# Kernel tuning notes

Measured on AMD Instinct MI355X. Metric: run time of the kernel, lower is better.

Reference implementation:

```python
import jax, jax.numpy as jnp
import numpy as np

B, T, C = 2, 2048, 2048
N_HEAD, N_KV_HEAD = 16, 4
HEAD_DIM = C // N_HEAD  # 128
EPS = 1e-6


def rms_norm(x):
    # no learned scale, normalize over head_dim (last axis)
    return x * jax.lax.rsqrt(jnp.mean(jnp.square(x), axis=-1, keepdims=True) + EPS)


def apply_rotary_emb(x, cos, sin):
    # x: [B, T, H, D]; cos/sin: [T, D/2]  (rotate-half RoPE)
    x1, x2 = jnp.split(x, 2, axis=-1)
    c = cos[None, :, None, :]
    s = sin[None, :, None, :]
    return jnp.concatenate([x1 * c - x2 * s, x1 * s + x2 * c], axis=-1)


def setup_inputs() -> dict:
    key = jax.random.key(0)
    ks = jax.random.split(key, 6)
    x = jax.random.normal(ks[0], (B, T, C), dtype=jnp.float32)
    # real rotary tables: theta = 10000^{-2i/D}
    inv_freq = 1.0 / (10000.0 ** (jnp.arange(0, HEAD_DIM, 2, dtype=jnp.float32) / HEAD_DIM))
    angles = jnp.arange(T, dtype=jnp.float32)[:, None] * inv_freq[None, :]  # [T, D/2]
    cos, sin = jnp.cos(angles), jnp.sin(angles)
    std = 0.02
    Wq = jax.random.normal(ks[1], (C, N_HEAD * HEAD_DIM), dtype=jnp.float32) * std
    Wk = jax.random.normal(ks[2], (C, N_KV_HEAD * HEAD_DIM), dtype=jnp.float32) * std
    Wv = jax.random.normal(ks[3], (C, N_KV_HEAD * HEAD_DIM), dtype=jnp.float32) * std
    Wp = jax.random.normal(ks[4], (C, C), dtype=jnp.float32) * std
    return {"x": x, "cos": cos, "sin": sin, "Wq": Wq, "Wk": Wk, "Wv": Wv, "Wp": Wp}


def reference(x, cos, sin, Wq, Wk, Wv, Wp):
    Bx, Tx, Cx = x.shape
    q = (x @ Wq).reshape(Bx, Tx, N_HEAD, HEAD_DIM)
    k = (x @ Wk).reshape(Bx, Tx, N_KV_HEAD, HEAD_DIM)
    v = (x @ Wv).reshape(Bx, Tx, N_KV_HEAD, HEAD_DIM)
    q = rms_norm(apply_rotary_emb(q, cos, sin))
    k = rms_norm(apply_rotary_emb(k, cos, sin))
    # module scales q by 1/sqrt(D) AND nn.dot_product_attention scales again
    q = q * (1.0 / jnp.sqrt(HEAD_DIM))
    # GQA head repeat
    n_rep = N_HEAD // N_KV_HEAD
    k = jnp.repeat(k, n_rep, axis=2)  # [B, T, H, D]
    v = jnp.repeat(v, n_rep, axis=2)
    scores = jnp.einsum("bthd,bshd->bhts", q, k) / jnp.sqrt(jnp.asarray(HEAD_DIM, x.dtype))
    causal = jnp.tril(jnp.ones((Tx, Tx), dtype=bool))  # key <= query
    scores = jnp.where(causal[None, None, :, :], scores, jnp.finfo(scores.dtype).min)
    probs = jax.nn.softmax(scores, axis=-1)
    y = jnp.einsum("bhts,bshd->bthd", probs, v).reshape(Bx, Tx, Cx)
    return y @ Wp
```

## Files before the change

### kernel.cpp

```cpp
#include <hip/hip_runtime.h>
#include <hip/hip_bf16.h>
#include <math.h>

#define B_  2
#define T_  2048
#define C_  2048
#define NH_ 16
#define NKV_ 4
#define HD_ 128
#define NREP_ (NH_/NKV_)

#define QKVLD 3072
#define KOFF  2048
#define VOFF  2560

#define QSCALE 0.01127105500694502f

#if defined(__has_builtin)
# if __has_builtin(__builtin_amdgcn_exp2f)
#  define EXP2F(x) __builtin_amdgcn_exp2f(x)
# else
#  define EXP2F(x) exp2f(x)
# endif
#else
# define EXP2F(x) exp2f(x)
#endif

typedef __bf16 bf16x8 __attribute__((ext_vector_type(8)));
typedef float  f32x4  __attribute__((ext_vector_type(4)));
typedef float  f32x16 __attribute__((ext_vector_type(16)));

__device__ inline void gload_lds16(const void* g, void* l) {
    __builtin_amdgcn_global_load_lds((const __attribute__((address_space(1))) void*)g,
                                     (__attribute__((address_space(3))) void*)l, 16, 0, 0);
}

__global__ __launch_bounds__(256) void prep(const float* __restrict__ x,
                                            const float* __restrict__ Wq,
                                            const float* __restrict__ Wk,
                                            const float* __restrict__ Wv,
                                            const float* __restrict__ Wp,
                                            __bf16* __restrict__ xb,
                                            __bf16* __restrict__ wqkvT,
                                            __bf16* __restrict__ wpT)
{
    __shared__ float tl[32][33];
    const int bx  = blockIdx.x;
    const int tid = threadIdx.x;

    if (bx < 4096) {
        size_t i = ((size_t)bx * 256 + tid) * 8;
        float4 a = *(const float4*)&x[i];
        float4 b = *(const float4*)&x[i + 4];
        union { __bf16 h[8]; uint4 u; } pk;
        pk.h[0] = (__bf16)a.x; pk.h[1] = (__bf16)a.y; pk.h[2] = (__bf16)a.z; pk.h[3] = (__bf16)a.w;
        pk.h[4] = (__bf16)b.x; pk.h[5] = (__bf16)b.y; pk.h[6] = (__bf16)b.z; pk.h[7] = (__bf16)b.w;
        *(uint4*)&xb[i] = pk.u;
        return;
    }

    const float* src;
    int ncols, c0, dr0, k0;
    if (bx < 10240) {
        int r  = bx - 4096;
        int ct = r % 96;
        k0 = (r / 96) * 32;
        if (ct < 64)      { src = Wq; ncols = 2048; c0 = ct * 32;        dr0 = ct * 32; }
        else if (ct < 80) { src = Wk; ncols = 512;  c0 = (ct - 64) * 32; dr0 = KOFF + (ct - 64) * 32; }
        else              { src = Wv; ncols = 512;  c0 = (ct - 80) * 32; dr0 = VOFF + (ct - 80) * 32; }
    } else {
        int r  = bx - 10240;
        src = Wp; ncols = 2048;
        c0  = (r & 63) * 32; dr0 = c0;
        k0  = (r >> 6) * 32;
    }
    __bf16* dst = (bx < 10240) ? wqkvT : wpT;

    int rr = tid >> 3;
    int c4 = (tid & 7) * 4;
    float4 v = *(const float4*)&src[(size_t)(k0 + rr) * ncols + c0 + c4];
    tl[rr][c4] = v.x; tl[rr][c4 + 1] = v.y; tl[rr][c4 + 2] = v.z; tl[rr][c4 + 3] = v.w;
    __syncthreads();
    union { __bf16 h[4]; uint2 u; } pk;
#pragma unroll
    for (int j = 0; j < 4; ++j) pk.h[j] = (__bf16)tl[c4 + j][rr];
    *(uint2*)&dst[(size_t)(dr0 + rr) * 2048 + k0 + c4] = pk.u;
}

template<typename TOUT>
__global__ __launch_bounds__(256) void gemm_bt(const __bf16* __restrict__ A,
                                               const __bf16* __restrict__ Bt,
                                               TOUT* __restrict__ C,
                                               int M, int N, int K, int ldc)
{
    __shared__ __bf16 As[2][128 * 32];
    __shared__ __bf16 Bs[2][128 * 32];

    const int tid  = threadIdx.x;
    const int wv   = tid >> 6;
    const int lane = tid & 63;
    const int grp  = lane >> 4;
    const int id16 = lane & 15;
    const int wr   = wv >> 1;
    const int wc   = wv & 1;

    const int row0 = blockIdx.y * 128;
    const int col0 = blockIdx.x * 128;

    const int sm = tid >> 2;
    const int sk = (tid & 3) << 3;

    const __bf16* ga0 = A  + (size_t)(row0 + sm) * K + sk;
    const __bf16* ga1 = A  + (size_t)(row0 + 64 + sm) * K + sk;
    const __bf16* gb0 = Bt + (size_t)(col0 + sm) * K + sk;
    const __bf16* gb1 = Bt + (size_t)(col0 + 64 + sm) * K + sk;

    f32x4 acc[4][4];
    const f32x4 fz = {0.f, 0.f, 0.f, 0.f};
#pragma unroll
    for (int i = 0; i < 4; ++i)
#pragma unroll
        for (int j = 0; j < 4; ++j) acc[i][j] = fz;

    const int nk = K >> 5;

    {
        __bf16* a0 = &As[0][wv << 9];
        __bf16* b0 = &Bs[0][wv << 9];
        gload_lds16(ga0, a0);
        gload_lds16(ga1, a0 + 2048);
        gload_lds16(gb0, b0);
        gload_lds16(gb1, b0 + 2048);
    }

    for (int kt = 0; kt < nk; ++kt) {
        const int bufc = kt & 1;
        asm volatile("s_waitcnt vmcnt(0)" ::: "memory");
        __syncthreads();

        if (kt + 1 < nk) {
            const int kb = (kt + 1) << 5;
            __bf16* a0 = &As[1 - bufc][wv << 9];
            __bf16* b0 = &Bs[1 - bufc][wv << 9];
            gload_lds16(ga0 + kb, a0);
            gload_lds16(ga1 + kb, a0 + 2048);
            gload_lds16(gb0 + kb, b0);
            gload_lds16(gb1 + kb, b0 + 2048);
        }

        bf16x8 af[4], bfr[4];
#pragma unroll
        for (int i = 0; i < 4; ++i)
            af[i] = *(const bf16x8*)&As[bufc][((wr << 6) + (i << 4) + id16) * 32 + (grp << 3)];
#pragma unroll
        for (int j = 0; j < 4; ++j)
            bfr[j] = *(const bf16x8*)&Bs[bufc][((wc << 6) + (j << 4) + id16) * 32 + (grp << 3)];
#pragma unroll
        for (int i = 0; i < 4; ++i)
#pragma unroll
            for (int j = 0; j < 4; ++j)
                acc[i][j] = __builtin_amdgcn_mfma_f32_16x16x32_bf16(af[i], bfr[j], acc[i][j], 0, 0, 0);
    }

#pragma unroll
    for (int i = 0; i < 4; ++i) {
        int gr = row0 + (wr << 6) + (i << 4) + (grp << 2);
#pragma unroll
        for (int j = 0; j < 4; ++j) {
            int gc = col0 + (wc << 6) + (j << 4) + id16;
#pragma unroll
            for (int r = 0; r < 4; ++r) {
                if constexpr (sizeof(TOUT) == 4)
                    C[(size_t)(gr + r) * ldc + gc] = acc[i][j][r];
                else
                    C[(size_t)(gr + r) * ldc + gc] = (TOUT)acc[i][j][r];
            }
        }
    }
}

__global__ __launch_bounds__(256) void rope_vt(__bf16* __restrict__ qkv,
                                               const float* __restrict__ cosb,
                                               const float* __restrict__ sinb,
                                               __bf16* __restrict__ vt)
{
    __shared__ __bf16 tl[32][HD_ + 8];
    const int bx  = blockIdx.x;
    const int tid = threadIdx.x;

    if (bx < 20480) {
        int gw   = bx * 4 + (tid >> 6);
        int lane = tid & 63;
        int bt = gw / 20;
        int hd = gw % 20;
        int t  = bt & (T_ - 1);
        float scale = (hd < 16) ? QSCALE : 1.0f;

        __bf16* p = qkv + (size_t)bt * QKVLD + hd * HD_;
        float c = cosb[t * 64 + lane];
        float s = sinb[t * 64 + lane];
        float x1 = (float)p[lane];
        float x2 = (float)p[lane + 64];
        float r1 = x1 * c - x2 * s;
        float r2 = x1 * s + x2 * c;
        float ss = r1 * r1 + r2 * r2;
#pragma unroll
        for (int off = 32; off; off >>= 1) ss += __shfl_xor(ss, off, 64);
        float inv = rsqrtf(ss * (1.f / 128.f) + 1e-6f) * scale;
        p[lane]      = (__bf16)(r1 * inv);
        p[lane + 64] = (__bf16)(r2 * inv);
        return;
    }
    {
        int vbx = bx - 20480;
        int st  = vbx & 63;
        int bkv = vbx >> 6;
        int b = bkv >> 2, kv = bkv & 3;
        int s0 = st << 5;
        {
            int s = tid >> 3;
            int d = (tid & 7) << 4;
            const __bf16* src = qkv + (size_t)(b * T_ + s0 + s) * QKVLD + VOFF + kv * HD_ + d;
            *(bf16x8*)&tl[s][d]     = *(const bf16x8*)src;
            *(bf16x8*)&tl[s][d + 8] = *(const bf16x8*)(src + 8);
        }
        __syncthreads();
        {
            int d  = tid >> 1;
            int sh = (tid & 1) << 4;
            __bf16 tmp[16];
#pragma unroll
            for (int j = 0; j < 16; ++j) tmp[j] = tl[sh + j][d];
            __bf16* dst = vt + ((size_t)(b * NKV_ + kv) * HD_ + d) * T_ + s0 + sh;
            *(bf16x8*)dst       = *(bf16x8*)&tmp[0];
            *(bf16x8*)(dst + 8) = *(bf16x8*)&tmp[8];
        }
    }
}

__global__ __launch_bounds__(256, 2) void attn32(const __bf16* __restrict__ qkv,
                                                 const __bf16* __restrict__ vbT,
                                                 __bf16* __restrict__ y,
                                                 float* __restrict__ pOA,
                                                 float* __restrict__ pOB,
                                                 float* __restrict__ pLA,
                                                 float* __restrict__ pLB)
{
    __shared__ __bf16 Ks[2][64 * 128];
    __shared__ __bf16 Vs[2][64 * 128];

    const int tid  = threadIdx.x;
    const int wv   = tid >> 6;
    const int lane = tid & 63;
    const int l31  = lane & 31;
    const int h32  = lane >> 5;

    const int bx   = blockIdx.x;
    const int b    = (bx >> 2) & 1;
    const int kv   = bx & 3;
    const int m    = bx >> 3;
    const int hh   = m & 3;
    const int role = (m >> 2) & 1;
    const int p    = m >> 3;
    const int h    = kv * 4 + hh;
    const int bh   = b * 16 + h;
    const int slot = p * 32 + bh;

    const int hi  = 15 - p;
    const int lo  = p;
    const int tts = role ? (15 - 2 * p) : 99;

    auto KT = [&](int t) { return role ? (t < tts ? 17 + t : t - tts) : t; };

    int qw0 = hi * 128 + wv * 32;
    int qme = qw0 + l31;

    uint koff[4], voff[4];
#pragma unroll
    for (int i = 0; i < 4; ++i) {
        int r  = (wv * 4 + i) * 4 + (lane >> 4);
        int c  = lane & 15;
        int cs = c ^ (r & 15);
        koff[i] = (uint)(r * (QKVLD * 2) + cs * 16);
        int d   = r + ((cs >> 3) << 6);
        voff[i] = (uint)(d * (T_ * 2) + (cs & 7) * 16);
    }
    const char* kg = (const char*)(qkv + (size_t)b * T_ * QKVLD + KOFF + kv * HD_);
    const char* vg = (const char*)(vbT + ((size_t)(b * NKV_ + kv) * HD_) * T_);

    uint off8[8];
#pragma unroll
    for (int s = 0; s < 8; ++s)
        off8[s] = (uint)(l31 * 256 + ((((s << 1) + h32) ^ (l31 & 15)) << 4));

#define STAGE(BUF, KN)                                                        \
    {                                                                         \
        const char* kp = kg + (size_t)(KN) * (64 * QKVLD * 2);                \
        const char* vp = vg + (size_t)(KN) * (64 * 2);                        \
        __bf16* kl = &Ks[BUF][(wv * 4) * 512];                                \
        __bf16* vl = &Vs[BUF][(wv * 4) * 512];                                \
        _Pragma("unroll")                                                     \
        for (int i = 0; i < 4; ++i) gload_lds16(kp + koff[i], kl + i * 512);  \
        _Pragma("unroll")                                                     \
        for (int i = 0; i < 4; ++i) gload_lds16(vp + voff[i], vl + i * 512);  \
    }

    bf16x8 qf[8], qf2[8];
    {
        const __bf16* qp = qkv + (size_t)(b * T_ + hi * 128 + wv * 32 + l31) * QKVLD + h * HD_ + h32 * 8;
#pragma unroll
        for (int s = 0; s < 8; ++s) qf[s] = *(const bf16x8*)(qp + s * 16);
        const __bf16* qp2 = qkv + (size_t)(b * T_ + lo * 128 + wv * 32 + l31) * QKVLD + h * HD_ + h32 * 8;
#pragma unroll
        for (int s = 0; s < 8; ++s) qf2[s] = *(const bf16x8*)(qp2 + s * 16);
    }

    f32x16 o[4];
#pragma unroll
    for (int dt = 0; dt < 4; ++dt)
#pragma unroll
        for (int r = 0; r < 16; ++r) o[dt][r] = 0.f;
    float l_p = 0.f;

#define STORE_PARTIAL(PO, PL)                                                   \
    {                                                                           \
        float lsum = l_p + __shfl_xor(l_p, 32, 64);                             \
        int qloc = wv * 32 + l31;                                               \
        float* po = (PO) + ((size_t)slot * 128 + qloc) * 128;                   \
        _Pragma("unroll")                                                       \
        for (int dt = 0; dt < 4; ++dt)                                          \
            _Pragma("unroll")                                                   \
            for (int g = 0; g < 4; ++g) {                                       \
                float4 f = {o[dt][4 * g + 0], o[dt][4 * g + 1],                 \
                            o[dt][4 * g + 2], o[dt][4 * g + 3]};                \
                *(float4*)&po[dt * 32 + 8 * g + 4 * h32] = f;                   \
            }                                                                   \
        if (h32 == 0) (PL)[slot * 128 + qloc] = lsum;                           \
    }

#define TILE_BODY(TT, BUFC)                                                     \
    {                                                                           \
        const int tt_ = (TT);                                                   \
        asm volatile("s_waitcnt vmcnt(0)" ::: "memory");                        \
        __syncthreads();                                                        \
        if (tt_ + 1 < 17) { int kn_ = KT(tt_ + 1); STAGE(1 - (BUFC), kn_); }    \
        if (role && tt_ == tts) {                                               \
            STORE_PARTIAL(pOB, pLB);                                            \
            _Pragma("unroll")                                                   \
            for (int dt = 0; dt < 4; ++dt)                                      \
                _Pragma("unroll")                                               \
                for (int r = 0; r < 16; ++r) o[dt][r] = 0.f;                    \
            l_p = 0.f;                                                          \
            _Pragma("unroll")                                                   \
            for (int s = 0; s < 8; ++s) qf[s] = qf2[s];                         \
            qw0 = lo * 128 + wv * 32;                                           \
            qme = qw0 + l31;                                                    \
        }                                                                       \
        const int s0 = KT(tt_) << 6;                                            \
        if (s0 <= qw0 + 31) {                                                   \
            const char* Kb = (const char*)&Ks[BUFC][0];                         \
            const char* Vb = (const char*)&Vs[BUFC][0];                         \
            f32x16 S0, S1;                                                      \
            _Pragma("unroll")                                                   \
            for (int r = 0; r < 16; ++r) { S0[r] = 0.f; S1[r] = 0.f; }          \
            __builtin_amdgcn_s_setprio(1);                                      \
            _Pragma("unroll")                                                   \
            for (int s = 0; s < 8; ++s) {                                       \
                bf16x8 kf0 = *(const bf16x8*)(Kb + off8[s]);                    \
                bf16x8 kf1 = *(const bf16x8*)(Kb + off8[s] + 8192);             \
                S0 = __builtin_amdgcn_mfma_f32_32x32x16_bf16(kf0, qf[s], S0, 0, 0, 0); \
                S1 = __builtin_amdgcn_mfma_f32_32x32x16_bf16(kf1, qf[s], S1, 0, 0, 0); \
            }                                                                   \
            __builtin_amdgcn_s_setprio(0);                                      \
            const bool domask = (s0 + 63 > qw0);                                \
            uint w[16];                                                         \
            _Pragma("unroll")                                                   \
            for (int i = 0; i < 8; ++i) {                                       \
                const int r0 = 2 * i;                                           \
                float e0 = EXP2F(S0[r0]);                                       \
                float e1 = EXP2F(S0[r0 + 1]);                                   \
                if (domask) {                                                   \
                    int k0 = s0 + (r0 & 3) + 8 * (r0 >> 2) + 4 * h32;           \
                    if (k0     > qme) e0 = 0.f;                                 \
                    if (k0 + 1 > qme) e1 = 0.f;                                 \
                }                                                               \
                l_p += e0 + e1;                                                 \
                union { __bf16 h2[2]; uint u; } pk;                             \
                pk.h2[0] = (__bf16)e0; pk.h2[1] = (__bf16)e1;                   \
                w[i] = pk.u;                                                    \
            }                                                                   \
            _Pragma("unroll")                                                   \
            for (int i = 0; i < 8; ++i) {                                       \
                const int r0 = 2 * i;                                           \
                float e0 = EXP2F(S1[r0]);                                       \
                float e1 = EXP2F(S1[r0 + 1]);                                   \
                if (domask) {                                                   \
                    int k0 = s0 + 32 + (r0 & 3) + 8 * (r0 >> 2) + 4 * h32;      \
                    if (k0     > qme) e0 = 0.f;                                 \
                    if (k0 + 1 > qme) e1 = 0.f;                                 \
                }                                                               \
                l_p += e0 + e1;                                                 \
                union { __bf16 h2[2]; uint u; } pk;                             \
                pk.h2[0] = (__bf16)e0; pk.h2[1] = (__bf16)e1;                   \
                w[8 + i] = pk.u;                                                \
            }                                                                   \
            union U8 { uint u[4]; bf16x8 v; };                                  \
            bf16x8 pf[4];                                                       \
            _Pragma("unroll")                                                   \
            for (int ks = 0; ks < 4; ++ks) {                                    \
                const int bsel = ((ks >> 1) << 3) + ((ks & 1) << 2);            \
                uint a0 = w[bsel],     b0 = w[bsel + 2];                        \
                uint a1 = w[bsel + 1], b1 = w[bsel + 3];                        \
                asm("v_permlane32_swap_b32 %0, %1" : "+v"(a0), "+v"(b0));       \
                asm("v_permlane32_swap_b32 %0, %1" : "+v"(a1), "+v"(b1));       \
                U8 t;                                                           \
                t.u[0] = a0; t.u[1] = a1; t.u[2] = b0; t.u[3] = b1;             \
                pf[ks] = t.v;                                                   \
            }                                                                   \
            __builtin_amdgcn_s_setprio(1);                                      \
            _Pragma("unroll")                                                   \
            for (int dt = 0; dt < 4; ++dt) {                                    \
                const int ab = (dt >> 1) << 2;                                  \
                const int hf = (dt & 1) * 8192;                                 \
                _Pragma("unroll")                                               \
                for (int ks = 0; ks < 4; ++ks) {                                \
                    bf16x8 vf = *(const bf16x8*)(Vb + off8[ab + ks] + hf);      \
                    o[dt] = __builtin_amdgcn_mfma_f32_32x32x16_bf16(vf, pf[ks], o[dt], 0, 0, 0); \
                }                                                               \
            }                                                                   \
            __builtin_amdgcn_s_setprio(0);                                      \
        }                                                                       \
    }

    STAGE(0, KT(0));

    for (int tt = 0; tt < 16; tt += 2) {
        TILE_BODY(tt, 0);
        TILE_BODY(tt + 1, 1);
    }
    TILE_BODY(16, 0);

    if (role == 0) {
        STORE_PARTIAL(pOA, pLA);
    } else {
        float l  = l_p + __shfl_xor(l_p, 32, 64);
        float inv = 1.f / l;
        __bf16* yp = y + (size_t)(b * T_ + qw0 + l31) * C_ + h * HD_;
#pragma unroll
        for (int dt = 0; dt < 4; ++dt)
#pragma unroll
            for (int g = 0; g < 4; ++g) {
                union { __bf16 h4[4]; uint2 u; } pk;
#pragma unroll
                for (int e = 0; e < 4; ++e) pk.h4[e] = (__bf16)(o[dt][4 * g + e] * inv);
                *(uint2*)&yp[dt * 32 + 8 * g + 4 * h32] = pk.u;
            }
    }
#undef TILE_BODY
#undef STORE_PARTIAL
#undef STAGE
}

__global__ __launch_bounds__(256) void attn_combine(const float* __restrict__ pOA,
                                                    const float* __restrict__ pOB,
                                                    const float* __restrict__ pLA,
                                                    const float* __restrict__ pLB,
                                                    __bf16* __restrict__ y)
{
    int slot = blockIdx.x;
    int p  = slot >> 5, bh = slot & 31;
    int b  = bh >> 4,   h  = bh & 15;
    int hi = 15 - p;
    int t  = threadIdx.x;
    int q  = t >> 1;
    int dh = (t & 1) << 6;

    float inv = 1.f / (pLA[slot * 128 + q] + pLB[slot * 128 + q]);
    size_t base = ((size_t)slot * 128 + q) * 128 + dh;
    __bf16* yp = y + (size_t)(b * T_ + hi * 128 + q) * C_ + h * HD_ + dh;
#pragma unroll
    for (int d0 = 0; d0 < 64; d0 += 8) {
        float4 a0 = *(const float4*)&pOA[base + d0];
        float4 a1 = *(const float4*)&pOA[base + d0 + 4];
        float4 b0 = *(const float4*)&pOB[base + d0];
        float4 b1 = *(const float4*)&pOB[base + d0 + 4];
        union { __bf16 h8[8]; uint4 u; } pk;
        pk.h8[0] = (__bf16)((a0.x + b0.x) * inv);
        pk.h8[1] = (__bf16)((a0.y + b0.y) * inv);
        pk.h8[2] = (__bf16)((a0.z + b0.z) * inv);
        pk.h8[3] = (__bf16)((a0.w + b0.w) * inv);
        pk.h8[4] = (__bf16)((a1.x + b1.x) * inv);
        pk.h8[5] = (__bf16)((a1.y + b1.y) * inv);
        pk.h8[6] = (__bf16)((a1.z + b1.z) * inv);
        pk.h8[7] = (__bf16)((a1.w + b1.w) * inv);
        *(uint4*)&yp[d0] = pk.u;
    }
}

extern "C" void kernel_launch(void* const* d_in, const int* in_sizes, int n_in,
                              void* d_out, int out_size, void* d_ws, size_t ws_size,
                              hipStream_t stream)
{
    const float* x    = (const float*)d_in[0];
    const float* cosb = (const float*)d_in[1];
    const float* sinb = (const float*)d_in[2];
    const float* Wq   = (const float*)d_in[3];
    const float* Wk   = (const float*)d_in[4];
    const float* Wv   = (const float*)d_in[5];
    const float* Wp   = (const float*)d_in[6];
    float* out = (float*)d_out;

    const int M = B_ * T_;

    char* w = (char*)d_ws;
    __bf16* xb    = (__bf16*)w;  w += (size_t)M * C_ * 2;
    __bf16* qkv   = (__bf16*)w;  w += (size_t)M * QKVLD * 2;
    __bf16* wqkvT = (__bf16*)w;  w += (size_t)QKVLD * C_ * 2;
    __bf16* wpT   = (__bf16*)w;  w += (size_t)C_ * C_ * 2;
    __bf16* vt    = (__bf16*)w;  w += (size_t)M * NKV_ * HD_ * 2;
    __bf16* y     = (__bf16*)w;  w += (size_t)M * C_ * 2;
    float*  pOB   = (float*)w;
    float*  pOA   = (float*)xb;
    float*  pLA   = (float*)wqkvT;
    float*  pLB   = pLA + 8 * 32 * 128;

    prep<<<14336, 256, 0, stream>>>(x, Wq, Wk, Wv, Wp, xb, wqkvT, wpT);

    gemm_bt<__bf16><<<dim3(QKVLD / 128, M / 128), 256, 0, stream>>>(xb, wqkvT, qkv, M, QKVLD, C_, QKVLD);

    rope_vt<<<20992, 256, 0, stream>>>(qkv, cosb, sinb, vt);

    attn32<<<512, 256, 0, stream>>>(qkv, vt, y, pOA, pOB, pLA, pLB);
    attn_combine<<<256, 256, 0, stream>>>(pOA, pOB, pLA, pLB, y);

    gemm_bt<float><<<dim3(C_ / 128, M / 128), 256, 0, stream>>>(y, wpT, out, M, C_, C_, C_);
}
```

Before: 310.3 us.

## Use 256x256-tile GEMM with 8 waves for the QKV projection

Adds a new bf16 MFMA GEMM kernel with 256x256 output tiles, K-step 64, 512 threads, double-buffered direct global-to-LDS loads, and an XOR-swizzled LDS layout. The QKV projection now launches this kernel in place of the 128x128 tile kernel. The larger tile raises arithmetic intensity and cuts global traffic per FLOP. The cost is a much smaller grid (12x16 = 192 blocks on a GPU with many CUs, so under one wave) and one block per CU because of the heavy LDS and register use.

```diff
diff --git a/kernel.cpp b/kernel.cpp
--- a/kernel.cpp
+++ b/kernel.cpp
@@ -85,6 +85,124 @@
 #pragma unroll
     for (int j = 0; j < 4; ++j) pk.h[j] = (__bf16)tl[c4 + j][rr];
     *(uint2*)&dst[(size_t)(dr0 + rr) * 2048 + k0 + c4] = pk.u;
+}
+
+template<typename TOUT>
+__global__ __launch_bounds__(512, 1) void gemm256(const __bf16* __restrict__ A,
+                                                  const __bf16* __restrict__ Bt,
+                                                  TOUT* __restrict__ C,
+                                                  int M, int N, int K, int ldc)
+{
+    __shared__ __bf16 As[2][256 * 64];
+    __shared__ __bf16 Bs[2][256 * 64];
+
+    const int tid  = threadIdx.x;
+    const int wv   = tid >> 6;
+    const int lane = tid & 63;
+    const int grp  = lane >> 4;
+    const int id16 = lane & 15;
+    const int wr   = wv >> 2;
+    const int wc   = wv & 3;
+
+    const int row0 = blockIdx.y * 256;
+    const int col0 = blockIdx.x * 256;
+
+    const int srow = lane >> 3;
+    const int cs16 = (((lane & 7) ^ srow) << 4);
+    const __bf16* gA = A  + (size_t)(row0 + wv * 8 + srow) * K;
+    const __bf16* gB = Bt + (size_t)(col0 + wv * 8 + srow) * K;
+
+    const int aBase = (wr * 128 + id16) * 64;
+    const int bBase = (wc * 64  + id16) * 64;
+    int physe[2];
+#pragma unroll
+    for (int ks = 0; ks < 2; ++ks)
+        physe[ks] = (((ks << 2) + grp) ^ (id16 & 7)) << 3;
+
+    f32x4 acc[8][4];
+    const f32x4 fz = {0.f, 0.f, 0.f, 0.f};
+#pragma unroll
+    for (int i = 0; i < 8; ++i)
+#pragma unroll
+        for (int j = 0; j < 4; ++j) acc[i][j] = fz;
+
+    const int NK = K >> 6;
+
+#define STAGE256(BUF, KT)                                                      \
+    {                                                                          \
+        const int kb_ = (KT) << 6;                                             \
+        _Pragma("unroll")                                                      \
+        for (int i = 0; i < 4; ++i)                                            \
+            gload_lds16((const char*)(gA + (size_t)i * 64 * K + kb_) + cs16,   \
+                        &As[BUF][(i * 64 + wv * 8) * 64]);                     \
+        _Pragma("unroll")                                                      \
+        for (int i = 0; i < 4; ++i)                                            \
+            gload_lds16((const char*)(gB + (size_t)i * 64 * K + kb_) + cs16,   \
+                        &Bs[BUF][(i * 64 + wv * 8) * 64]);                     \
+    }
+
+#define TILE256(KT, BUF)                                                       \
+    {                                                                          \
+        if ((KT) == NK - 1) { asm volatile("s_waitcnt vmcnt(0)" ::: "memory"); } \
+        else                { asm volatile("s_waitcnt vmcnt(8)" ::: "memory"); } \
+        __builtin_amdgcn_s_barrier();                                          \
+        _Pragma("unroll")                                                      \
+        for (int p = 0; p < 4; ++p) {                                          \
+            const int mh = p >> 1, nq = p & 1;                                 \
+            bf16x8 af[4][2], bfv[2][2];                                        \
+            _Pragma("unroll")                                                  \
+            for (int s = 0; s < 4; ++s)                                        \
+                _Pragma("unroll")                                              \
+                for (int ks = 0; ks < 2; ++ks)                                 \
+                    af[s][ks] = *(const bf16x8*)&As[BUF][aBase + (mh * 4 + s) * 1024 + physe[ks]]; \
+            _Pragma("unroll")                                                  \
+            for (int s = 0; s < 2; ++s)                                        \
+                _Pragma("unroll")                                              \
+                for (int ks = 0; ks < 2; ++ks)                                 \
+                    bfv[s][ks] = *(const bf16x8*)&Bs[BUF][bBase + (nq * 2 + s) * 1024 + physe[ks]]; \
+            __builtin_amdgcn_s_setprio(1);                                     \
+            _Pragma("unroll")                                                  \
+            for (int s = 0; s < 4; ++s)                                        \
+                _Pragma("unroll")                                              \
+                for (int n = 0; n < 2; ++n)                                    \
+                    _Pragma("unroll")                                          \
+                    for (int ks = 0; ks < 2; ++ks)                             \
+                        acc[mh * 4 + s][nq * 2 + n] =                          \
+                            __builtin_amdgcn_mfma_f32_16x16x32_bf16(af[s][ks], bfv[n][ks], \
+                                                                    acc[mh * 4 + s][nq * 2 + n], 0, 0, 0); \
+            __builtin_amdgcn_s_setprio(0);                                     \
+            __builtin_amdgcn_s_barrier();                                      \
+        }                                                                      \
+        asm volatile("s_waitcnt lgkmcnt(0)" ::: "memory");                     \
+        __builtin_amdgcn_s_barrier();                                          \
+        if ((KT) + 2 < NK) STAGE256(BUF, (KT) + 2);                            \
+    }
+
+    STAGE256(0, 0);
+    STAGE256(1, 1);
+
+    for (int kt = 0; kt < NK; kt += 2) {
+        TILE256(kt, 0);
+        TILE256(kt + 1, 1);
+    }
+
+#pragma unroll
+    for (int mf = 0; mf < 8; ++mf) {
+        int gr = row0 + wr * 128 + mf * 16 + grp * 4;
+#pragma unroll
+        for (int nf = 0; nf < 4; ++nf) {
+            int gc = col0 + wc * 64 + nf * 16 + id16;
+#pragma unroll
+            for (int r = 0; r < 4; ++r) {
+                if constexpr (sizeof(TOUT) == 4)
+                    C[(size_t)(gr + r) * ldc + gc] = acc[mf][nf][r];
+                else
+                    C[(size_t)(gr + r) * ldc + gc] = (TOUT)acc[mf][nf][r];
+            }
+        }
+    }
+#undef TILE256
+#undef STAGE256
 }
 
 template<typename TOUT>
@@ -526,7 +644,7 @@
 
     prep<<<14336, 256, 0, stream>>>(x, Wq, Wk, Wv, Wp, xb, wqkvT, wpT);
 
-    gemm_bt<__bf16><<<dim3(QKVLD / 128, M / 128), 256, 0, stream>>>(xb, wqkvT, qkv, M, QKVLD, C_, QKVLD);
+    gemm256<__bf16><<<dim3(QKVLD / 256, M / 256), 512, 0, stream>>>(xb, wqkvT, qkv, M, QKVLD, C_, QKVLD);
 
     rope_vt<<<20992, 256, 0, stream>>>(qkv, cosb, sinb, vt);
 
```

Result: slower. 323.1 us (+4.1%).

## Use 256x256-tile 4-stage pipelined GEMM for QKV projection

Applied to the files above, without the earlier changes.

Adds a new GEMM kernel with 256x256 output tiles, 512 threads, a 4-deep LDS buffer ring fed by direct global-to-LDS loads, and XCD-aware block remapping, and uses it for the QKV projection. The aim is more data reuse per tile and better hiding of memory latency than the 128x128 double-buffered kernel. It uses much more LDS and registers, so only one workgroup fits per CU, and the grid shrinks to 192 blocks, which may underfill the CUs.

```diff
diff --git a/kernel.cpp b/kernel.cpp
--- a/kernel.cpp
+++ b/kernel.cpp
@@ -85,6 +85,132 @@
 #pragma unroll
     for (int j = 0; j < 4; ++j) pk.h[j] = (__bf16)tl[c4 + j][rr];
     *(uint2*)&dst[(size_t)(dr0 + rr) * 2048 + k0 + c4] = pk.u;
+}
+
+template<typename TOUT>
+__global__ __launch_bounds__(512, 1) void gemm256(const __bf16* __restrict__ A,
+                                                  const __bf16* __restrict__ Bt,
+                                                  TOUT* __restrict__ C,
+                                                  int M, int N, int K, int ldc,
+                                                  int nbx)
+{
+    __shared__ __bf16 As[4][256 * 32];
+    __shared__ __bf16 Bs[4][256 * 32];
+
+    const int tid  = threadIdx.x;
+    const int wv   = tid >> 6;
+    const int lane = tid & 63;
+    const int grp  = lane >> 4;
+    const int id16 = lane & 15;
+    const int wr   = wv >> 2;
+    const int wc   = wv & 3;
+
+    const int nwg  = gridDim.x;
+    const int cpx  = nwg >> 3;
+    const int bid  = blockIdx.x;
+    const int wg   = (bid & 7) * cpx + (bid >> 3);
+    const int row0 = (wg / nbx) * 256;
+    const int col0 = (wg % nbx) * 256;
+
+    uint soff[2];
+#pragma unroll
+    for (int l = 0; l < 2; ++l) {
+        int r = (wv * 2 + l) * 16 + (lane >> 2);
+        int c = (lane & 3) ^ ((r ^ (r >> 2)) & 3);
+        soff[l] = (uint)(r * (K * 2) + c * 16);
+    }
+    const char* gA = (const char*)(A  + (size_t)row0 * K);
+    const char* gB = (const char*)(Bt + (size_t)col0 * K);
+
+    uint aoff[8], boff[4];
+#pragma unroll
+    for (int mf = 0; mf < 8; ++mf) {
+        int r = wr * 128 + mf * 16 + id16;
+        aoff[mf] = (uint)(r * 64 + ((grp ^ ((r ^ (r >> 2)) & 3)) << 4));
+    }
+#pragma unroll
+    for (int nf = 0; nf < 4; ++nf) {
+        int r = wc * 64 + nf * 16 + id16;
+        boff[nf] = (uint)(r * 64 + ((grp ^ ((r ^ (r >> 2)) & 3)) << 4));
+    }
+
+    f32x4 acc[8][4];
+    const f32x4 fz = {0.f, 0.f, 0.f, 0.f};
+#pragma unroll
+    for (int i = 0; i < 8; ++i)
+#pragma unroll
+        for (int j = 0; j < 4; ++j) acc[i][j] = fz;
+
+    const int NK = K >> 5;
+
+#define STG(BUF, KT, L)                                                        \
+    {                                                                          \
+        gload_lds16(gA + (size_t)(KT) * 64 + soff[L], &As[BUF][(wv * 2 + (L)) * 512]); \
+        gload_lds16(gB + (size_t)(KT) * 64 + soff[L], &Bs[BUF][(wv * 2 + (L)) * 512]); \
+    }
+
+#define TILE32(KT, BUF)                                                        \
+    {                                                                          \
+        if ((KT) + 3 <= NK)      { asm volatile("s_waitcnt vmcnt(8)" ::: "memory"); } \
+        else if ((KT) + 2 == NK) { asm volatile("s_waitcnt vmcnt(4)" ::: "memory"); } \
+        else                     { asm volatile("s_waitcnt vmcnt(0)" ::: "memory"); } \
+        __builtin_amdgcn_s_barrier();                                          \
+        const char* Ab = (const char*)&As[BUF][0];                             \
+        const char* Bb = (const char*)&Bs[BUF][0];                             \
+        _Pragma("unroll")                                                      \
+        for (int p = 0; p < 2; ++p) {                                          \
+            bf16x8 af[4], bfv[4];                                              \
+            _Pragma("unroll")                                                  \
+            for (int s = 0; s < 4; ++s)                                        \
+                af[s] = *(const bf16x8*)(Ab + aoff[p * 4 + s]);                \
+            _Pragma("unroll")                                                  \
+            for (int n = 0; n < 4; ++n)                                        \
+                bfv[n] = *(const bf16x8*)(Bb + boff[n]);                       \
+            if ((KT) + 3 < NK) { STG((((BUF) + 3) & 3), (KT) + 3, p) }         \
+            __builtin_amdgcn_s_barrier();                                      \
+            asm volatile("s_waitcnt lgkmcnt(0)" ::: "memory");                 \
+            __builtin_amdgcn_s_setprio(1);                                     \
+            _Pragma("unroll")                                                  \
+            for (int s = 0; s < 4; ++s)                                        \
+                _Pragma("unroll")                                              \
+                for (int n = 0; n < 4; ++n)                                    \
+                    acc[p * 4 + s][n] =                                        \
+                        __builtin_amdgcn_mfma_f32_16x16x32_bf16(af[s], bfv[n], \
+                                                                acc[p * 4 + s][n], 0, 0, 0); \
+            __builtin_amdgcn_s_setprio(0);                                     \
+        }                                                                      \
+    }
+
+#pragma unroll
+    for (int t = 0; t < 3; ++t) {
+        STG(t, t, 0)
+        STG(t, t, 1)
+    }
+
+    for (int kt = 0; kt < NK; kt += 4) {
+        TILE32(kt,     0);
+        TILE32(kt + 1, 1);
+        TILE32(kt + 2, 2);
+        TILE32(kt + 3, 3);
+    }
+
+#pragma unroll
+    for (int mf = 0; mf < 8; ++mf) {
+        int gr = row0 + wr * 128 + mf * 16 + grp * 4;
+#pragma unroll
+        for (int nf = 0; nf < 4; ++nf) {
+            int gc = col0 + wc * 64 + nf * 16 + id16;
+#pragma unroll
+            for (int r = 0; r < 4; ++r) {
+                if constexpr (sizeof(TOUT) == 4)
+                    C[(size_t)(gr + r) * ldc + gc] = acc[mf][nf][r];
+                else
+                    C[(size_t)(gr + r) * ldc + gc] = (TOUT)acc[mf][nf][r];
+            }
+        }
+    }
+#undef TILE32
+#undef STG
 }
 
 template<typename TOUT>
@@ -526,7 +652,7 @@
 
     prep<<<14336, 256, 0, stream>>>(x, Wq, Wk, Wv, Wp, xb, wqkvT, wpT);
 
-    gemm_bt<__bf16><<<dim3(QKVLD / 128, M / 128), 256, 0, stream>>>(xb, wqkvT, qkv, M, QKVLD, C_, QKVLD);
+    gemm256<__bf16><<<192, 512, 0, stream>>>(xb, wqkvT, qkv, M, QKVLD, C_, QKVLD, QKVLD / 256);
 
     rope_vt<<<20992, 256, 0, stream>>>(qkv, cosb, sinb, vt);
 
```

Measured after the change: 312.7 us. No clear change (+0.8%).
